# Performance work log

Hardware: AMD Instinct MI355X
Metric: run time of the kernel (lower is better)

Reference implementation:

```python
import jax, jax.numpy as jnp
import numpy as np
import math

D_MODEL = 1024
NUM_HEADS = 16


def setup_inputs() -> dict:
    key = jax.random.key(0)
    ks = jax.random.split(key, 5)
    B, S, D = 4, 2048, D_MODEL
    scale = 1.0 / math.sqrt(D)
    x = jax.random.normal(ks[0], (B, S, D), dtype=jnp.float32)
    wq = jax.random.normal(ks[1], (D, D), dtype=jnp.float32) * scale
    wk = jax.random.normal(ks[2], (D, D), dtype=jnp.float32) * scale
    wv = jax.random.normal(ks[3], (D, D), dtype=jnp.float32) * scale
    wo = jax.random.normal(ks[4], (D, D), dtype=jnp.float32) * scale
    return {"x": x, "wq": wq, "wk": wk, "wv": wv, "wo": wo}


def _mhsa(x, wq, wk, wv, wo):
    B, S, D = x.shape
    H = NUM_HEADS
    dk = D // H
    # projections: y = x @ W^T
    q = (x @ wq.T).reshape(B, S, H, dk).transpose(0, 2, 1, 3)  # [B,H,S,dk]
    k = (x @ wk.T).reshape(B, S, H, dk).transpose(0, 2, 1, 3)
    v = (x @ wv.T).reshape(B, S, H, dk).transpose(0, 2, 1, 3)
    scores = jnp.einsum("bhqd,bhkd->bhqk", q, k) / jnp.sqrt(jnp.asarray(dk, x.dtype))
    mask = jnp.tril(jnp.ones((S, S), dtype=bool))  # [S,S] causal
    neg_inf = jnp.asarray(-jnp.inf, scores.dtype)
    scores_masked = jnp.where(mask, scores, neg_inf)
    max_scores = jnp.max(scores_masked, axis=-1, keepdims=True)
    max_scores = jnp.where(jnp.isfinite(max_scores), max_scores, jnp.zeros_like(max_scores))
    exp_scores = jnp.exp(scores - max_scores) * mask.astype(scores.dtype)
    denom = jnp.maximum(exp_scores.sum(axis=-1, keepdims=True), 1e-9)
    attn = exp_scores / denom
    out = jnp.einsum("bhqk,bhkd->bhqd", attn, v)  # [B,H,S,dk]
    out = out.transpose(0, 2, 1, 3).reshape(B, S, D)
    return out @ wo.T


def reference(x, wq, wk, wv, wo):
    return _mhsa(x, wq, wk, wv, wo)
```

## Files before the change

### kernel.cpp

```cpp
#include <hip/hip_runtime.h>
#include <stdint.h>


typedef __attribute__((ext_vector_type(8))) short short8;
typedef __attribute__((ext_vector_type(4))) short short4v;
typedef __attribute__((ext_vector_type(4))) float float4v;

#define EXP_C1 0.18033688011112042f
#define EXP_C2 5.770780163555852f

__device__ inline short f2bf(float f) {
  union { float f; uint32_t u; } v; v.f = f;
  uint32_t r = (v.u + 0x7fffu + ((v.u >> 16) & 1)) >> 16;
  return (short)(uint16_t)r;
}

__device__ inline void async_copy16(const void* g, void* l) {
  __builtin_amdgcn_global_load_lds(
      (const __attribute__((address_space(1))) void*)g,
      (__attribute__((address_space(3))) void*)l, 16, 0, 0);
}

__global__ __launch_bounds__(256) void cvt(const float* __restrict__ s,
                                           short* __restrict__ d, int n4) {
  const int i = blockIdx.x * 256 + threadIdx.x;
  if (i < n4) {
    const float4v v = *(const float4v*)(s + 4 * (size_t)i);
    short4v o;
    o[0] = f2bf(v[0]); o[1] = f2bf(v[1]);
    o[2] = f2bf(v[2]); o[3] = f2bf(v[3]);
    *(short4v*)(d + 4 * (size_t)i) = o;
  }
}

template <int MODE>
__global__ __launch_bounds__(256) void gemm_bt(
    const short* __restrict__ A,
    const short* __restrict__ W0, const short* __restrict__ W1,
    const short* __restrict__ W2,
    short* __restrict__ Yb0, short* __restrict__ Yb1, short* __restrict__ Yb2,
    float* __restrict__ Yf) {
  constexpr int Kd = 1024;
  __shared__ __align__(16) short As[128 * 32];
  __shared__ __align__(16) short Bs[128 * 32];

  const int t = threadIdx.x;
  const int w = t >> 6, l = t & 63, l15 = l & 15, quad = l >> 4;
  const int wm = w >> 1, wn = w & 1;
  const int m0 = blockIdx.y * 128, n0 = blockIdx.x * 128;

  const short* W = W0;
  short* Yb = Yb0;
  if (MODE == 0) {
    if (blockIdx.z == 1) { W = W1; Yb = Yb1; }
    else if (blockIdx.z == 2) { W = W2; Yb = Yb2; }
  }

  float4v acc[4][4];
#pragma unroll
  for (int i = 0; i < 4; i++)
#pragma unroll
    for (int j = 0; j < 4; j++) acc[i][j] = (float4v){0.f, 0.f, 0.f, 0.f};

  const int r4 = t >> 2, c48 = (t & 3) * 8;
  const short* Wbase = W + (n0 + r4) * Kd + c48;
  short* AsW = &As[w * 512];
  short* BsW = &Bs[w * 512];
  const int i0 = m0 + r4;
  const int i1 = m0 + 64 + r4;

  for (int k0 = 0; k0 < Kd; k0 += 32) {
    if (MODE == 0) {
      async_copy16(A + (size_t)i0 * Kd + k0 + c48, AsW);
      async_copy16(A + (size_t)i1 * Kd + k0 + c48, AsW + 2048);
    } else {
      const int k = k0 + c48, h = k >> 6, dd = k & 63;
      async_copy16(A + ((((size_t)(i0 >> 11) * 16 + h) * 2048 + (i0 & 2047)) * 64 + dd), AsW);
      async_copy16(A + ((((size_t)(i1 >> 11) * 16 + h) * 2048 + (i1 & 2047)) * 64 + dd), AsW + 2048);
    }
    async_copy16(Wbase + k0, BsW);
    async_copy16(Wbase + 64 * Kd + k0, BsW + 2048);
    __syncthreads();
    short8 af[4], bf[4];
#pragma unroll
    for (int mi = 0; mi < 4; mi++)
      af[mi] = *(const short8*)&As[(wm * 64 + mi * 16 + l15) * 32 + quad * 8];
#pragma unroll
    for (int ni = 0; ni < 4; ni++)
      bf[ni] = *(const short8*)&Bs[(wn * 64 + ni * 16 + l15) * 32 + quad * 8];
#pragma unroll
    for (int mi = 0; mi < 4; mi++)
#pragma unroll
      for (int ni = 0; ni < 4; ni++)
        acc[mi][ni] = __builtin_amdgcn_mfma_f32_16x16x32_bf16(
            af[mi], bf[ni], acc[mi][ni], 0, 0, 0);
    __syncthreads();
  }

#pragma unroll
  for (int mi = 0; mi < 4; mi++) {
    const int ib = m0 + wm * 64 + mi * 16 + quad * 4;
#pragma unroll
    for (int ni = 0; ni < 4; ni++) {
      const int j = n0 + wn * 64 + ni * 16 + l15;
#pragma unroll
      for (int r = 0; r < 4; r++) {
        const int i = ib + r;
        if (MODE == 0) {
          Yb[((((size_t)(i >> 11) * 16 + (j >> 6)) * 2048 + (i & 2047)) * 64 + (j & 63))] =
              f2bf(acc[mi][ni][r]);
        } else {
          Yf[(size_t)i * 1024 + j] = acc[mi][ni][r];
        }
      }
    }
  }
}

__global__ __launch_bounds__(256) void transV(const short* __restrict__ V,
                                              short* __restrict__ VT) {
  __shared__ __align__(16) short Ls[64 * 72];
  const int t = threadIdx.x;
  const int s0 = blockIdx.x * 64, bh = blockIdx.y;
  const short* Vh = V + (size_t)bh * 2048 * 64;
  short* Th = VT + (size_t)bh * 64 * 2048;
  const int r = t >> 2, c = (t & 3) * 16;
  *(short8*)&Ls[r * 72 + c] = *(const short8*)&Vh[(size_t)(s0 + r) * 64 + c];
  *(short8*)&Ls[r * 72 + c + 8] = *(const short8*)&Vh[(size_t)(s0 + r) * 64 + c + 8];
  __syncthreads();
  short8 o0, o1;
#pragma unroll
  for (int j = 0; j < 8; j++) {
    o0[j] = Ls[(c + j) * 72 + r];
    o1[j] = Ls[(c + 8 + j) * 72 + r];
  }
  *(short8*)&Th[(size_t)r * 2048 + s0 + c] = o0;
  *(short8*)&Th[(size_t)r * 2048 + s0 + c + 8] = o1;
}

__global__ __launch_bounds__(256) void attn2(
    short* __restrict__ Q,
    const short* __restrict__ K,
    const short* __restrict__ VT) {
  __shared__ __align__(16) short Ks[64 * 72];
  __shared__ __align__(16) short Vs[64 * 72];
  __shared__ __align__(16) short Ps[4 * 16 * 72];

  const int t = threadIdx.x;
  const int w = t >> 6, l = t & 63, l15 = l & 15, quad = l >> 4;
  const int bh = blockIdx.y;
  short* Qh = Q + (size_t)bh * 2048 * 64;
  const short* Kh = K + (size_t)bh * 2048 * 64;
  const short* Vh = VT + (size_t)bh * 64 * 2048;
  const int sr = t >> 2, scc = (t & 3) * 16;
  short* PsW = &Ps[w * 16 * 72];

  short8 ones;
#pragma unroll
  for (int j = 0; j < 8; j++) ones[j] = (short)0x3F80;

  for (int pass = 0; pass < 2; pass++) {
    const int q0 = (pass ? (31 - blockIdx.x) : blockIdx.x) * 64;
    const int kmax = q0 + 64;
    const int qrow = q0 + w * 16 + l15;
    const short8 qf0 = *(const short8*)&Qh[(size_t)qrow * 64 + quad * 8];
    const short8 qf1 = *(const short8*)&Qh[(size_t)qrow * 64 + 32 + quad * 8];

    float4v acc[4];
#pragma unroll
    for (int dt = 0; dt < 4; dt++) acc[dt] = (float4v){0.f, 0.f, 0.f, 0.f};
    float4v accL = (float4v){0.f, 0.f, 0.f, 0.f};

    short8 kv0 = *(const short8*)&Kh[(size_t)sr * 64 + scc];
    short8 kv1 = *(const short8*)&Kh[(size_t)sr * 64 + scc + 8];
    short8 vv0 = *(const short8*)&Vh[(size_t)sr * 2048 + scc];
    short8 vv1 = *(const short8*)&Vh[(size_t)sr * 2048 + scc + 8];

    for (int kb = 0; kb < kmax; kb += 64) {
      *(short8*)&Ks[sr * 72 + scc] = kv0;
      *(short8*)&Ks[sr * 72 + scc + 8] = kv1;
      *(short8*)&Vs[sr * 72 + scc] = vv0;
      *(short8*)&Vs[sr * 72 + scc + 8] = vv1;
      __syncthreads();

      const int kb2 = (kb + 64 < kmax) ? kb + 64 : kb;
      kv0 = *(const short8*)&Kh[(size_t)(kb2 + sr) * 64 + scc];
      kv1 = *(const short8*)&Kh[(size_t)(kb2 + sr) * 64 + scc + 8];
      vv0 = *(const short8*)&Vh[(size_t)sr * 2048 + kb2 + scc];
      vv1 = *(const short8*)&Vh[(size_t)sr * 2048 + kb2 + scc + 8];

      float4v sv[4];
#pragma unroll
      for (int kt = 0; kt < 4; kt++) {
        const short8 kf0 = *(const short8*)&Ks[(kt * 16 + l15) * 72 + quad * 8];
        const short8 kf1 = *(const short8*)&Ks[(kt * 16 + l15) * 72 + 32 + quad * 8];
        float4v s = (float4v){0.f, 0.f, 0.f, 0.f};
        s = __builtin_amdgcn_mfma_f32_16x16x32_bf16(qf0, kf0, s, 0, 0, 0);
        s = __builtin_amdgcn_mfma_f32_16x16x32_bf16(qf1, kf1, s, 0, 0, 0);
        sv[kt] = s;
      }

#pragma unroll
      for (int kt = 0; kt < 4; kt++)
#pragma unroll
        for (int ri = 0; ri < 4; ri++) {
          const int key = kb + kt * 16 + l15;
          const int qg = q0 + w * 16 + quad * 4 + ri;
          float p = __builtin_amdgcn_exp2f(sv[kt][ri] * EXP_C1 - EXP_C2);
          p = (key <= qg) ? p : 0.f;
          const int row = quad * 4 + ri, col = kt * 16 + l15;
          PsW[row * 72 + (((col >> 3) ^ ((row >> 3) & 1)) << 3) + (col & 7)] =
              f2bf(p);
        }
      __builtin_amdgcn_wave_barrier();

      const int swl = (l15 >> 3) & 1;
      const short8 pf0 = *(const short8*)&PsW[l15 * 72 + ((quad ^ swl) << 3)];
      const short8 pf1 = *(const short8*)&PsW[l15 * 72 + (((4 + quad) ^ swl) << 3)];
#pragma unroll
      for (int dt = 0; dt < 4; dt++) {
        const short8 vf0 = *(const short8*)&Vs[(dt * 16 + l15) * 72 + quad * 8];
        const short8 vf1 = *(const short8*)&Vs[(dt * 16 + l15) * 72 + 32 + quad * 8];
        acc[dt] = __builtin_amdgcn_mfma_f32_16x16x32_bf16(pf0, vf0, acc[dt], 0, 0, 0);
        acc[dt] = __builtin_amdgcn_mfma_f32_16x16x32_bf16(pf1, vf1, acc[dt], 0, 0, 0);
      }
      accL = __builtin_amdgcn_mfma_f32_16x16x32_bf16(pf0, ones, accL, 0, 0, 0);
      accL = __builtin_amdgcn_mfma_f32_16x16x32_bf16(pf1, ones, accL, 0, 0, 0);
      __syncthreads();
    }

#pragma unroll
    for (int ri = 0; ri < 4; ri++) {
      const int qg = q0 + w * 16 + quad * 4 + ri;
      const float inv = 1.0f / fmaxf(accL[ri], 1e-30f);
#pragma unroll
      for (int dt = 0; dt < 4; dt++)
        Qh[(size_t)qg * 64 + dt * 16 + l15] = f2bf(acc[dt][ri] * inv);
    }
  }
}

extern "C" void kernel_launch(void* const* d_in, const int* in_sizes, int n_in,
                              void* d_out, int out_size, void* d_ws,
                              size_t ws_size, hipStream_t stream) {
  const float* x = (const float*)d_in[0];
  const float* wq = (const float*)d_in[1];
  const float* wk = (const float*)d_in[2];
  const float* wv = (const float*)d_in[3];
  const float* wo = (const float*)d_in[4];
  float* out = (float*)d_out;

  short* xb = (short*)d_out;
  short* vtg = xb + (size_t)8192 * 1024;

  short* wqb = (short*)d_ws;
  short* wkb = wqb + (size_t)1024 * 1024;
  short* wvb = wkb + (size_t)1024 * 1024;
  short* wob = wvb + (size_t)1024 * 1024;
  short* qws = wob + (size_t)1024 * 1024;
  short* kws = qws + (size_t)8192 * 1024;
  short* vws = kws + (size_t)8192 * 1024;

  cvt<<<8192, 256, 0, stream>>>(x, xb, 2097152);
  cvt<<<1024, 256, 0, stream>>>(wq, wqb, 262144);
  cvt<<<1024, 256, 0, stream>>>(wk, wkb, 262144);
  cvt<<<1024, 256, 0, stream>>>(wv, wvb, 262144);
  cvt<<<1024, 256, 0, stream>>>(wo, wob, 262144);

  gemm_bt<0><<<dim3(8, 64, 3), 256, 0, stream>>>(
      xb, wqb, wkb, wvb, qws, kws, vws, nullptr);
  transV<<<dim3(32, 64), 256, 0, stream>>>(vws, vtg);
  attn2<<<dim3(16, 64), 256, 0, stream>>>(qws, kws, vtg);
  gemm_bt<1><<<dim3(8, 64, 1), 256, 0, stream>>>(
      qws, wob, nullptr, nullptr, nullptr, nullptr, nullptr, out);
}
```

Measured before the change: 295.9 us.

## Transpose attention MFMA operands, mask only diagonal tile, merge weight conversions

Swaps the A/B operands of the score and PV MFMAs so that each lane holds a query column. P can then be written to LDS as packed 4-element vectors instead of scattered scalar stores, and the output is written with vector stores. The causal mask is applied only on the diagonal key block, and the separate exp pass over a score array is folded into the score loop. The four weight-conversion launches are merged into one kernel launch to cut launch overhead. The swizzle on P writes is dropped, so LDS bank conflicts on the reads could change.

```diff
diff --git a/kernel.cpp b/kernel.cpp
--- a/kernel.cpp
+++ b/kernel.cpp
@@ -31,6 +31,23 @@
     o[2] = f2bf(v[2]); o[3] = f2bf(v[3]);
     *(short4v*)(d + 4 * (size_t)i) = o;
   }
+}
+
+__global__ __launch_bounds__(256) void cvtW(
+    const float* __restrict__ a, const float* __restrict__ b,
+    const float* __restrict__ c, const float* __restrict__ e,
+    short* __restrict__ oa, short* __restrict__ ob,
+    short* __restrict__ oc, short* __restrict__ oe) {
+  const float* s = (blockIdx.y == 0) ? a : (blockIdx.y == 1) ? b
+                   : (blockIdx.y == 2) ? c : e;
+  short* d = (blockIdx.y == 0) ? oa : (blockIdx.y == 1) ? ob
+             : (blockIdx.y == 2) ? oc : oe;
+  const int i = blockIdx.x * 256 + threadIdx.x;
+  const float4v v = *(const float4v*)(s + 4 * (size_t)i);
+  short4v o;
+  o[0] = f2bf(v[0]); o[1] = f2bf(v[1]);
+  o[2] = f2bf(v[2]); o[3] = f2bf(v[3]);
+  *(short4v*)(d + 4 * (size_t)i) = o;
 }
 
 template <int MODE>
@@ -138,7 +155,7 @@
   *(short8*)&Th[(size_t)r * 2048 + s0 + c + 8] = o1;
 }
 
-__global__ __launch_bounds__(256) void attn2(
+__global__ __launch_bounds__(256) void attn3(
     short* __restrict__ Q,
     const short* __restrict__ K,
     const short* __restrict__ VT) {
@@ -161,10 +178,9 @@
 
   for (int pass = 0; pass < 2; pass++) {
     const int q0 = (pass ? (31 - blockIdx.x) : blockIdx.x) * 64;
-    const int kmax = q0 + 64;
-    const int qrow = q0 + w * 16 + l15;
-    const short8 qf0 = *(const short8*)&Qh[(size_t)qrow * 64 + quad * 8];
-    const short8 qf1 = *(const short8*)&Qh[(size_t)qrow * 64 + 32 + quad * 8];
+    const int qn = q0 + w * 16 + l15;
+    const short8 qf0 = *(const short8*)&Qh[(size_t)qn * 64 + quad * 8];
+    const short8 qf1 = *(const short8*)&Qh[(size_t)qn * 64 + 32 + quad * 8];
 
     float4v acc[4];
 #pragma unroll
@@ -176,66 +192,65 @@
     short8 vv0 = *(const short8*)&Vh[(size_t)sr * 2048 + scc];
     short8 vv1 = *(const short8*)&Vh[(size_t)sr * 2048 + scc + 8];
 
-    for (int kb = 0; kb < kmax; kb += 64) {
+    for (int kb = 0; kb <= q0; kb += 64) {
+      const bool diag = (kb == q0);
       *(short8*)&Ks[sr * 72 + scc] = kv0;
       *(short8*)&Ks[sr * 72 + scc + 8] = kv1;
       *(short8*)&Vs[sr * 72 + scc] = vv0;
       *(short8*)&Vs[sr * 72 + scc + 8] = vv1;
       __syncthreads();
 
-      const int kb2 = (kb + 64 < kmax) ? kb + 64 : kb;
+      const int kb2 = diag ? kb : kb + 64;
       kv0 = *(const short8*)&Kh[(size_t)(kb2 + sr) * 64 + scc];
       kv1 = *(const short8*)&Kh[(size_t)(kb2 + sr) * 64 + scc + 8];
       vv0 = *(const short8*)&Vh[(size_t)sr * 2048 + kb2 + scc];
       vv1 = *(const short8*)&Vh[(size_t)sr * 2048 + kb2 + scc + 8];
 
-      float4v sv[4];
 #pragma unroll
       for (int kt = 0; kt < 4; kt++) {
         const short8 kf0 = *(const short8*)&Ks[(kt * 16 + l15) * 72 + quad * 8];
         const short8 kf1 = *(const short8*)&Ks[(kt * 16 + l15) * 72 + 32 + quad * 8];
         float4v s = (float4v){0.f, 0.f, 0.f, 0.f};
-        s = __builtin_amdgcn_mfma_f32_16x16x32_bf16(qf0, kf0, s, 0, 0, 0);
-        s = __builtin_amdgcn_mfma_f32_16x16x32_bf16(qf1, kf1, s, 0, 0, 0);
-        sv[kt] = s;
+        s = __builtin_amdgcn_mfma_f32_16x16x32_bf16(kf0, qf0, s, 0, 0, 0);
+        s = __builtin_amdgcn_mfma_f32_16x16x32_bf16(kf1, qf1, s, 0, 0, 0);
+        short4v pw;
+        if (diag) {
+#pragma unroll
+          for (int ri = 0; ri < 4; ri++) {
+            const int key = kb + kt * 16 + quad * 4 + ri;
+            const float p = __builtin_amdgcn_exp2f(s[ri] * EXP_C1 - EXP_C2);
+            pw[ri] = f2bf((key <= qn) ? p : 0.f);
+          }
+        } else {
+#pragma unroll
+          for (int ri = 0; ri < 4; ri++)
+            pw[ri] = f2bf(__builtin_amdgcn_exp2f(s[ri] * EXP_C1 - EXP_C2));
+        }
+        *(short4v*)&PsW[l15 * 72 + kt * 16 + quad * 4] = pw;
       }
-
-#pragma unroll
-      for (int kt = 0; kt < 4; kt++)
-#pragma unroll
-        for (int ri = 0; ri < 4; ri++) {
-          const int key = kb + kt * 16 + l15;
-          const int qg = q0 + w * 16 + quad * 4 + ri;
-          float p = __builtin_amdgcn_exp2f(sv[kt][ri] * EXP_C1 - EXP_C2);
-          p = (key <= qg) ? p : 0.f;
-          const int row = quad * 4 + ri, col = kt * 16 + l15;
-          PsW[row * 72 + (((col >> 3) ^ ((row >> 3) & 1)) << 3) + (col & 7)] =
-              f2bf(p);
-        }
       __builtin_amdgcn_wave_barrier();
 
-      const int swl = (l15 >> 3) & 1;
-      const short8 pf0 = *(const short8*)&PsW[l15 * 72 + ((quad ^ swl) << 3)];
-      const short8 pf1 = *(const short8*)&PsW[l15 * 72 + (((4 + quad) ^ swl) << 3)];
+      const short8 pf0 = *(const short8*)&PsW[l15 * 72 + quad * 8];
+      const short8 pf1 = *(const short8*)&PsW[l15 * 72 + 32 + quad * 8];
 #pragma unroll
       for (int dt = 0; dt < 4; dt++) {
         const short8 vf0 = *(const short8*)&Vs[(dt * 16 + l15) * 72 + quad * 8];
         const short8 vf1 = *(const short8*)&Vs[(dt * 16 + l15) * 72 + 32 + quad * 8];
-        acc[dt] = __builtin_amdgcn_mfma_f32_16x16x32_bf16(pf0, vf0, acc[dt], 0, 0, 0);
-        acc[dt] = __builtin_amdgcn_mfma_f32_16x16x32_bf16(pf1, vf1, acc[dt], 0, 0, 0);
+        acc[dt] = __builtin_amdgcn_mfma_f32_16x16x32_bf16(vf0, pf0, acc[dt], 0, 0, 0);
+        acc[dt] = __builtin_amdgcn_mfma_f32_16x16x32_bf16(vf1, pf1, acc[dt], 0, 0, 0);
       }
-      accL = __builtin_amdgcn_mfma_f32_16x16x32_bf16(pf0, ones, accL, 0, 0, 0);
-      accL = __builtin_amdgcn_mfma_f32_16x16x32_bf16(pf1, ones, accL, 0, 0, 0);
+      accL = __builtin_amdgcn_mfma_f32_16x16x32_bf16(ones, pf0, accL, 0, 0, 0);
+      accL = __builtin_amdgcn_mfma_f32_16x16x32_bf16(ones, pf1, accL, 0, 0, 0);
       __syncthreads();
     }
 
-#pragma unroll
-    for (int ri = 0; ri < 4; ri++) {
-      const int qg = q0 + w * 16 + quad * 4 + ri;
-      const float inv = 1.0f / fmaxf(accL[ri], 1e-30f);
-#pragma unroll
-      for (int dt = 0; dt < 4; dt++)
-        Qh[(size_t)qg * 64 + dt * 16 + l15] = f2bf(acc[dt][ri] * inv);
+    const float inv = 1.0f / fmaxf(accL[0], 1e-30f);
+#pragma unroll
+    for (int dt = 0; dt < 4; dt++) {
+      short4v o;
+#pragma unroll
+      for (int ri = 0; ri < 4; ri++) o[ri] = f2bf(acc[dt][ri] * inv);
+      *(short4v*)&Qh[(size_t)qn * 64 + dt * 16 + quad * 4] = o;
     }
   }
 }
@@ -262,15 +277,12 @@
   short* vws = kws + (size_t)8192 * 1024;
 
   cvt<<<8192, 256, 0, stream>>>(x, xb, 2097152);
-  cvt<<<1024, 256, 0, stream>>>(wq, wqb, 262144);
-  cvt<<<1024, 256, 0, stream>>>(wk, wkb, 262144);
-  cvt<<<1024, 256, 0, stream>>>(wv, wvb, 262144);
-  cvt<<<1024, 256, 0, stream>>>(wo, wob, 262144);
+  cvtW<<<dim3(1024, 4), 256, 0, stream>>>(wq, wk, wv, wo, wqb, wkb, wvb, wob);
 
   gemm_bt<0><<<dim3(8, 64, 3), 256, 0, stream>>>(
       xb, wqb, wkb, wvb, qws, kws, vws, nullptr);
   transV<<<dim3(32, 64), 256, 0, stream>>>(vws, vtg);
-  attn2<<<dim3(16, 64), 256, 0, stream>>>(qws, kws, vtg);
+  attn3<<<dim3(16, 64), 256, 0, stream>>>(qws, kws, vtg);
   gemm_bt<1><<<dim3(8, 64, 1), 256, 0, stream>>>(
       qws, wob, nullptr, nullptr, nullptr, nullptr, nullptr, out);
 }
```

Result: faster. 282.0 us (-4.7%).
